# Kernel tuning notes

Measured on AMD Instinct MI355X. Metric: run time of the kernel, lower is better.

Reference implementation:

```python
import jax, jax.numpy as jnp
import numpy as np

B = 262144
L = 16      # latent_dim
H = 64      # hidden_dim
C = 8       # num_charts
O = 32      # output_dim
TAU_MIN = 0.01
TAU_DENOM_MIN = 0.001
EPS = 0.001
LN_EPS = 1e-5


def setup_inputs() -> dict:
    key = jax.random.key(0)
    ks = jax.random.split(key, 16)
    # latents kept well inside the Poincare ball
    z_geo = 0.1 * jax.random.normal(ks[0], (B, L), dtype=jnp.float32)
    z_tex = 0.1 * jax.random.normal(ks[1], (B, L), dtype=jnp.float32)
    def lin(k, fan_in, shape):
        bound = 1.0 / np.sqrt(fan_in)
        return jax.random.uniform(k, shape, jnp.float32, -bound, bound)
    chart_w = lin(ks[2], L, (C, H, L))   # stacked per-chart Linear weights
    chart_b = lin(ks[3], L, (C, H))
    router_w = lin(ks[4], L, (C, L))
    router_b = lin(ks[5], L, (C,))
    centers = 0.02 * jax.random.normal(ks[6], (C, L), dtype=jnp.float32)
    tex_w = lin(ks[7], L, (H, L))
    tex_b = lin(ks[8], L, (H,))
    ln_g = jnp.ones((H,), jnp.float32)
    ln_b = jnp.zeros((H,), jnp.float32)
    w1 = lin(ks[9], H, (H, H))
    b1 = lin(ks[10], H, (H,))
    w2 = lin(ks[11], H, (O, H))
    b2 = lin(ks[12], H, (O,))
    return dict(z_geo=z_geo, z_tex=z_tex, chart_w=chart_w, chart_b=chart_b,
                router_w=router_w, router_b=router_b, centers=centers,
                tex_w=tex_w, tex_b=tex_b, ln_g=ln_g, ln_b=ln_b,
                w1=w1, b1=b1, w2=w2, b2=b2)


def _temperature(z):
    r2 = jnp.sum(z * z, axis=-1)                      # [B]
    denom = jnp.maximum(1.0 - r2, TAU_DENOM_MIN)
    tau = (np.sqrt(L) * denom) * 0.5
    return jnp.maximum(tau, TAU_MIN)                  # [B]


def _gelu(x):
    return jax.nn.gelu(x, approximate=False)


def reference(z_geo, z_tex, chart_w, chart_b, router_w, router_b, centers,
              tex_w, tex_b, ln_g, ln_b, w1, b1, w2, b2):
    # hyperbolic distance scores  [B, C]
    diff = z_geo[:, None, :] - centers[None, :, :]
    dist_sq = jnp.sum(diff * diff, axis=-1)
    z_sq = jnp.sum(z_geo * z_geo, axis=-1, keepdims=True)   # [B,1]
    c_sq = jnp.sum(centers * centers, axis=-1)[None, :]      # [1,C]
    denom = (1.0 - z_sq) * (1.0 - c_sq)
    arg = 1.0 + 2.0 * dist_sq / (denom + EPS)
    dist = jnp.arccosh(jnp.maximum(arg, 1.0 + EPS))
    tau = _temperature(z_geo)                                # [B]
    scores = -dist / tau[:, None]
    scores = scores + 0.1 * (z_geo @ router_w.T + router_b) / tau[:, None]
    router_weights = jax.nn.softmax(scores, axis=-1)         # [B,C]

    # dense chart projection + weighted blend
    h_stack = jnp.einsum('bl,chl->bch', z_geo, chart_w) + chart_b[None]  # [B,C,H]
    h_global = jnp.sum(h_stack * router_weights[:, :, None], axis=1)     # [B,H]
    h_tex = z_tex @ tex_w.T + tex_b
    h = h_global + h_tex

    # renderer: LayerNorm -> GELU -> Linear -> GELU -> Linear
    mu = jnp.mean(h, axis=-1, keepdims=True)
    var = jnp.mean((h - mu) ** 2, axis=-1, keepdims=True)
    hn = (h - mu) * jax.lax.rsqrt(var + LN_EPS) * ln_g + ln_b
    h1 = _gelu(_gelu(hn) @ w1.T + b1)
    x_hat = h1 @ w2.T + b2
    return x_hat, router_weights
```

## Files before the change

### kernel.cpp

```cpp
#include <hip/hip_runtime.h>
#include <hip/hip_bf16.h>
#include <hip/hip_fp16.h>


typedef __attribute__((ext_vector_type(8))) short short8;
typedef __attribute__((ext_vector_type(4))) float f32x4;

__device__ __forceinline__ int pkbf2(float a, float b) {
    union { __hip_bfloat162 h2; int i; } u;
    u.h2 = __float22bfloat162_rn(make_float2(a, b));
    return u.i;
}
__device__ __forceinline__ short pkbf1(float a) { return (short)pkbf2(a, 0.f); }

__device__ __forceinline__ float gelu_fast(float x) {
    float x2 = x * x;
    float t  = __expf(fmaf(x2, 0.07135481f, 1.5957691f) * x);
    float r  = __builtin_amdgcn_rcpf(t + 1.0f);
    return fmaf(-x, r, x);
}
__device__ __forceinline__ int bpack(int k, int n, int KT) {
    return (((n >> 4) * KT + (k >> 5)) * 64 + (n & 15) + (((k & 31) >> 3) << 4)) * 8 + (k & 7);
}
__device__ __forceinline__ int gswz(int g) {
    return g ^ (((g >> 4) & 3) << 1) ^ ((g >> 3) & 1);
}
__device__ __forceinline__ short8 packrow8(const float* base) {
    const float4* p = (const float4*)base;
    float4 a = p[0], b = p[1];
    union { short8 s; int i[4]; } f;
    f.i[0] = pkbf2(a.x, a.y); f.i[1] = pkbf2(a.z, a.w);
    f.i[2] = pkbf2(b.x, b.y); f.i[3] = pkbf2(b.z, b.w);
    return f.s;
}

__global__ void pack_weights(const float* __restrict__ cw, const float* __restrict__ cb,
                             const float* __restrict__ txw, const float* __restrict__ txb,
                             const float* __restrict__ w1,  const float* __restrict__ w2,
                             const float* __restrict__ cen, const float* __restrict__ rb,
                             short* __restrict__ ws)
{
    const int tid = threadIdx.x;
    const int b = blockIdx.x;
    if (b < 40) {
        int idx = b * 256 + tid;
        int k = idx >> 6, n = idx & 63;
        float v;
        if (k < 128)       v = cw[(k >> 4) * 1024 + n * 16 + (k & 15)];
        else if (k < 144)  v = txw[n * 16 + (k - 128)];
        else if (k < 152)  v = cb[(k - 144) * 64 + n];
        else if (k == 152) v = txb[n];
        else               v = 0.f;
        ws[bpack(k, n, 5)] = pkbf1(v);
    } else if (b == 40) {
        for (int f = tid; f < 512; f += 256) {
            int lane = f & 63, e = f >> 6;
            int nt = e >> 1, kt = e & 1;
            int col = lane & 15, qq = lane >> 4;
            *(short8*)(ws + 10240 + f * 8) =
                packrow8(w1 + (nt * 16 + col) * 64 + kt * 32 + qq * 8);
        }
    } else if (b == 41) {
        int f = tid;
        int lane = f & 63, e = f >> 6;
        int nt = e >> 1, kt = e & 1;
        int col = lane & 15, qq = lane >> 4;
        *(short8*)(ws + 14336 + f * 8) =
            packrow8(w2 + (nt * 16 + col) * 64 + kt * 32 + qq * 8);
    } else {
        if (tid < 8) {
            float csq = 0.f;
            for (int l = 0; l < 16; l++) { float cv = cen[tid * 16 + l]; csq = fmaf(cv, cv, csq); }
            ((float4*)((char*)ws + 32768))[tid] =
                make_float4(csq, 1.0f - csq, 0.1f * rb[tid], 0.f);
        }
    }
}

constexpr int SCR_OFF = 20480;
constexpr int RS_OFF  = 28672;
constexpr int W2L_OFF = 32768;
constexpr int SMEM_SZ = 36864;

__global__ __launch_bounds__(256, 4) void topo_mfma(
    const float* __restrict__ zg,  const float* __restrict__ ztx,
    const float* __restrict__ cw,  const float* __restrict__ cb,
    const float* __restrict__ rw,  const float* __restrict__ rb,
    const float* __restrict__ cen, const float* __restrict__ txw,
    const float* __restrict__ txb, const float* __restrict__ lng,
    const float* __restrict__ lnb, const float* __restrict__ w1,
    const float* __restrict__ b1,  const float* __restrict__ w2,
    const float* __restrict__ b2,  const short* __restrict__ wsp,
    const int prepacked,
    float* __restrict__ out, int Btot)
{
    __shared__ __align__(16) char smem[SMEM_SZ];
    short* WA = (short*)smem;
    __half* RSh = (__half*)(smem + RS_OFF);
    const short8* W2L = (const short8*)(smem + W2L_OFF);

    const int tid = threadIdx.x;
    const int wv = tid >> 6, lane = tid & 63;
    const int q = lane >> 4, col = lane & 15;
    const int sub = (lane >> 3) & 1, j = lane & 7;

    if (prepacked) {
        const int4* src = (const int4*)wsp;
        int4* dst = (int4*)smem;
        #pragma unroll
        for (int i = 0; i < 5; i++) dst[i * 256 + tid] = src[i * 256 + tid];
        ((int4*)(smem + W2L_OFF))[tid] = ((const int4*)((const char*)wsp + 28672))[tid];
    } else {
        for (int idx = tid; idx < 160 * 64; idx += 256) {
            int k = idx >> 6, n = idx & 63;
            float v;
            if (k < 128)       v = cw[(k >> 4) * 1024 + n * 16 + (k & 15)];
            else if (k < 144)  v = txw[n * 16 + (k - 128)];
            else if (k < 152)  v = cb[(k - 144) * 64 + n];
            else if (k == 152) v = txb[n];
            else               v = 0.f;
            WA[bpack(k, n, 5)] = pkbf1(v);
        }
        {
            int e = tid >> 6, ln = tid & 63;
            int nt = e >> 1, kt = e & 1;
            *(short8*)(smem + W2L_OFF + (e * 64 + ln) * 16) =
                packrow8(w2 + (nt * 16 + (ln & 15)) * 64 + kt * 32 + (ln >> 4) * 8);
        }
    }

    const long sG = (long)blockIdx.x * 256 + tid;
    {
        float z[16];
        const float4* pg = (const float4*)(zg + sG * 16);
        #pragma unroll
        for (int v = 0; v < 4; v++) {
            float4 a = pg[v];
            z[v*4+0]=a.x; z[v*4+1]=a.y; z[v*4+2]=a.z; z[v*4+3]=a.w;
        }
        float r2 = 0.f;
        #pragma unroll
        for (int l = 0; l < 16; l++) r2 = fmaf(z[l], z[l], r2);
        const float inv_tau = __builtin_amdgcn_rcpf(fmaxf(2.0f * fmaxf(1.0f - r2, 0.001f), 0.01f));
        const float omr2 = 1.0f - r2;
        const float4* cvp = (const float4*)((const char*)wsp + 32768);
        float scv[8]; float smax = -1e30f;
        #pragma unroll
        for (int c = 0; c < 8; c++) {
            float csq, omc2, rb1;
            if (prepacked) {
                float4 kv = cvp[c]; csq = kv.x; omc2 = kv.y; rb1 = kv.z;
            } else {
                csq = 0.f;
                #pragma unroll
                for (int l = 0; l < 16; l++) { float cv = cen[c*16+l]; csq = fmaf(cv, cv, csq); }
                omc2 = 1.0f - csq; rb1 = 0.1f * rb[c];
            }
            const float4* cp = (const float4*)(cen + c * 16);
            const float4* rp = (const float4*)(rw  + c * 16);
            float zc = 0.f, dotv = 0.f;
            #pragma unroll
            for (int v = 0; v < 4; v++) {
                float4 cv = cp[v], rv = rp[v];
                zc   = fmaf(z[v*4+0],cv.x, fmaf(z[v*4+1],cv.y,
                       fmaf(z[v*4+2],cv.z, fmaf(z[v*4+3],cv.w, zc))));
                dotv = fmaf(z[v*4+0],rv.x, fmaf(z[v*4+1],rv.y,
                       fmaf(z[v*4+2],rv.z, fmaf(z[v*4+3],rv.w, dotv))));
            }
            float dsq = fmaf(-2.0f, zc, r2 + csq);
            float u = 2.0f * dsq * __builtin_amdgcn_rcpf(omr2 * omc2 + 0.001f);
            u = fmaxf(u, 0.001f);
            float dist  = __logf((1.0f + u) + __builtin_amdgcn_sqrtf(u * (u + 2.0f)));
            float score = (fmaf(0.1f, dotv, rb1) - dist) * inv_tau;
            scv[c] = score; smax = fmaxf(smax, score);
        }
        float esum = 0.f;
        #pragma unroll
        for (int c = 0; c < 8; c++) { scv[c] = __expf(scv[c] - smax); esum += scv[c]; }
        const float rinv = __builtin_amdgcn_rcpf(esum);
        union { ushort us[8]; int4 v; } hv;
        #pragma unroll
        for (int c = 0; c < 8; c++) {
            scv[c] *= rinv;
            hv.us[(c & 1) * 4 + (c >> 1)] = __half_as_ushort(__float2half_rn(scv[c]));
        }
        *(int4*)(RSh + tid * 8) = hv.v;
        float4* pr = (float4*)(out + (long)Btot * 32 + sG * 8);
        pr[0] = make_float4(scv[0], scv[1], scv[2], scv[3]);
        pr[1] = make_float4(scv[4], scv[5], scv[6], scv[7]);
    }

    short8 W1F[4][2];
    if (prepacked) {
        const short8* p1 = (const short8*)(wsp + 10240);
        #pragma unroll
        for (int nt = 0; nt < 4; nt++)
            #pragma unroll
            for (int kt = 0; kt < 2; kt++)
                W1F[nt][kt] = p1[(nt * 2 + kt) * 64 + lane];
    } else {
        const int kb = q * 8;
        #pragma unroll
        for (int nt = 0; nt < 4; nt++)
            #pragma unroll
            for (int kt = 0; kt < 2; kt++)
                W1F[nt][kt] = packrow8(w1 + (nt * 16 + col) * 64 + kt * 32 + kb);
    }
    float lngv[4], lnbv[4], b1v[4], b2v[2];
    #pragma unroll
    for (int nt = 0; nt < 4; nt++) {
        lngv[nt] = lng[nt * 16 + col];
        lnbv[nt] = lnb[nt * 16 + col];
        b1v[nt]  = b1[nt * 16 + col];
    }
    b2v[0] = b2[col]; b2v[1] = b2[16 + col];

    __syncthreads();

    short* scr = (short*)(smem + SCR_OFF) + wv * 1024;
    union Frag { short8 s; int i[4]; };

    const long blockBase = (long)blockIdx.x * 256;
    const float* zrow = zg  + (blockBase + wv * 64 + col) * 16 + ((q & 1) << 3);
    const float* trow = ztx + (blockBase + wv * 64 + col) * 16 + ((q & 1) << 3);

    float4 za = ((const float4*)zrow)[0], zb = ((const float4*)zrow)[1];
    float4 ta = ((const float4*)trow)[0], tb = ((const float4*)trow)[1];

    for (int t = 0; t < 4; t++) {
        const int  mBase = wv * 64 + t * 16;
        const int  sL = mBase + col;
        const int  rsb = sL * 8;

        float rc[4];
        {
            union { unsigned long long u; __half2 h[2]; } rr;
            rr.u = *(const unsigned long long*)(RSh + rsb + ((q >> 1) << 2));
            float2 f0 = __half22float2(rr.h[0]);
            float2 f1 = __half22float2(rr.h[1]);
            rc[0] = f0.x; rc[1] = f0.y; rc[2] = f1.x; rc[3] = f1.y;
        }

        f32x4 acc[4] = {{0.f,0.f,0.f,0.f},{0.f,0.f,0.f,0.f},{0.f,0.f,0.f,0.f},{0.f,0.f,0.f,0.f}};
        __builtin_amdgcn_s_setprio(1);
        #pragma unroll
        for (int kt = 0; kt < 4; kt++) {
            float r = rc[kt];
            Frag f;
            f.i[0] = pkbf2(r * za.x, r * za.y);
            f.i[1] = pkbf2(r * za.z, r * za.w);
            f.i[2] = pkbf2(r * zb.x, r * zb.y);
            f.i[3] = pkbf2(r * zb.z, r * zb.w);
            #pragma unroll
            for (int nt = 0; nt < 4; nt++) {
                short8 bf = *(const short8*)(WA + (nt * 5 + kt) * 512 + lane * 8);
                acc[nt] = __builtin_amdgcn_mfma_f32_16x16x32_bf16(f.s, bf, acc[nt], 0, 0, 0);
            }
        }
        {
            Frag f;
            if (q < 2) {
                f.i[0] = pkbf2(ta.x, ta.y); f.i[1] = pkbf2(ta.z, ta.w);
                f.i[2] = pkbf2(tb.x, tb.y); f.i[3] = pkbf2(tb.z, tb.w);
            } else if (q == 2) {
                union { int4 u; __half2 h[4]; } rv;
                rv.u = *(const int4*)(RSh + rsb);
                float2 e0 = __half22float2(rv.h[0]);
                float2 e1 = __half22float2(rv.h[1]);
                float2 e2 = __half22float2(rv.h[2]);
                float2 e3 = __half22float2(rv.h[3]);
                f.i[0] = pkbf2(e0.x, e2.x);
                f.i[1] = pkbf2(e0.y, e2.y);
                f.i[2] = pkbf2(e1.x, e3.x);
                f.i[3] = pkbf2(e1.y, e3.y);
            } else {
                f.i[0] = pkbf2(1.0f, 0.f); f.i[1] = 0; f.i[2] = 0; f.i[3] = 0;
            }
            #pragma unroll
            for (int nt = 0; nt < 4; nt++) {
                short8 bf = *(const short8*)(WA + (nt * 5 + 4) * 512 + lane * 8);
                acc[nt] = __builtin_amdgcn_mfma_f32_16x16x32_bf16(f.s, bf, acc[nt], 0, 0, 0);
            }
        }
        __builtin_amdgcn_s_setprio(0);

        if (t < 3) {
            const float4* pzn = (const float4*)(zrow + (t + 1) * 256);
            const float4* ptn = (const float4*)(trow + (t + 1) * 256);
            za = pzn[0]; zb = pzn[1]; ta = ptn[0]; tb = ptn[1];
        }

        float mu[4], rsd[4];
        #pragma unroll
        for (int reg = 0; reg < 4; reg++) {
            float a = acc[0][reg], b = acc[1][reg], c = acc[2][reg], d = acc[3][reg];
            float s  = (a + b) + (c + d);
            float s2 = fmaf(a, a, fmaf(b, b, fmaf(c, c, d * d)));
            s  += __shfl_xor(s, 1);  s  += __shfl_xor(s, 2);
            s  += __shfl_xor(s, 4);  s  += __shfl_xor(s, 8);
            s2 += __shfl_xor(s2, 1); s2 += __shfl_xor(s2, 2);
            s2 += __shfl_xor(s2, 4); s2 += __shfl_xor(s2, 8);
            float m = s * (1.0f / 64.0f);
            mu[reg]  = m;
            rsd[reg] = rsqrtf(fmaf(s2, 1.0f / 64.0f, -m * m) + 1e-5f);
        }

        #pragma unroll
        for (int nt = 0; nt < 4; nt++) {
            int high = (nt & 1) * 2 + sub;
            #pragma unroll
            for (int reg = 0; reg < 4; reg++) {
                float hn = (acc[nt][reg] - mu[reg]) * rsd[reg] * lngv[nt] + lnbv[nt];
                int grp = gswz((q * 4 + reg) + 16 * high);
                scr[(nt >> 1) * 512 + grp * 8 + j] = pkbf1(gelu_fast(hn));
            }
        }
        asm volatile("s_waitcnt lgkmcnt(0)" ::: "memory");

        short8 A2[2];
        {
            int grp = gswz(lane);
            A2[0] = *(const short8*)(scr +       grp * 8);
            A2[1] = *(const short8*)(scr + 512 + grp * 8);
        }

        #pragma unroll
        for (int nt = 0; nt < 4; nt++) {
            f32x4 a2 = {0.f, 0.f, 0.f, 0.f};
            __builtin_amdgcn_s_setprio(1);
            a2 = __builtin_amdgcn_mfma_f32_16x16x32_bf16(A2[0], W1F[nt][0], a2, 0, 0, 0);
            a2 = __builtin_amdgcn_mfma_f32_16x16x32_bf16(A2[1], W1F[nt][1], a2, 0, 0, 0);
            __builtin_amdgcn_s_setprio(0);
            int high = (nt & 1) * 2 + sub;
            #pragma unroll
            for (int reg = 0; reg < 4; reg++) {
                float h1v = gelu_fast(a2[reg] + b1v[nt]);
                int grp = gswz((q * 4 + reg) + 16 * high);
                scr[(nt >> 1) * 512 + grp * 8 + j] = pkbf1(h1v);
            }
        }
        asm volatile("s_waitcnt lgkmcnt(0)" ::: "memory");

        short8 A3[2];
        {
            int grp = gswz(lane);
            A3[0] = *(const short8*)(scr +       grp * 8);
            A3[1] = *(const short8*)(scr + 512 + grp * 8);
        }

        const long sOutBase = blockBase + mBase + q * 4;
        #pragma unroll
        for (int nt = 0; nt < 2; nt++) {
            f32x4 a3 = {0.f, 0.f, 0.f, 0.f};
            short8 wA = W2L[(nt * 2 + 0) * 64 + lane];
            short8 wB = W2L[(nt * 2 + 1) * 64 + lane];
            __builtin_amdgcn_s_setprio(1);
            a3 = __builtin_amdgcn_mfma_f32_16x16x32_bf16(A3[0], wA, a3, 0, 0, 0);
            a3 = __builtin_amdgcn_mfma_f32_16x16x32_bf16(A3[1], wB, a3, 0, 0, 0);
            __builtin_amdgcn_s_setprio(0);
            #pragma unroll
            for (int reg = 0; reg < 4; reg++)
                out[(sOutBase + reg) * 32 + nt * 16 + col] = a3[reg] + b2v[nt];
        }
    }
}

extern "C" void kernel_launch(void* const* d_in, const int* in_sizes, int n_in,
                              void* d_out, int out_size, void* d_ws, size_t ws_size,
                              hipStream_t stream) {
    const int B = in_sizes[0] / 16;
    const int prepacked = (d_ws != nullptr && ws_size >= 32896) ? 1 : 0;
    if (prepacked) {
        hipLaunchKernelGGL(pack_weights, dim3(43), dim3(256), 0, stream,
            (const float*)d_in[2],  (const float*)d_in[3],
            (const float*)d_in[7],  (const float*)d_in[8],
            (const float*)d_in[11], (const float*)d_in[13],
            (const float*)d_in[6],  (const float*)d_in[5],
            (short*)d_ws);
    }
    dim3 grid(B / 256), block(256);
    hipLaunchKernelGGL(topo_mfma, grid, block, 0, stream,
        (const float*)d_in[0],  (const float*)d_in[1],
        (const float*)d_in[2],  (const float*)d_in[3],
        (const float*)d_in[4],  (const float*)d_in[5],
        (const float*)d_in[6],  (const float*)d_in[7],
        (const float*)d_in[8],  (const float*)d_in[9],
        (const float*)d_in[10], (const float*)d_in[11],
        (const float*)d_in[12], (const float*)d_in[13],
        (const float*)d_in[14],
        (const short*)d_ws, prepacked,
        (float*)d_out, B);
}
```

Before: 138.9 us.

## Pass router weights via wave shuffles instead of LDS, raise occupancy to 5

Each thread keeps its packed fp16 router weights in registers, and the MFMA tile loop fetches them from the owning lane with __shfl instead of reading a shared-memory staging buffer. This removes 4 KB of LDS, so shared memory shrinks to 32 KB and launch bounds ask for 5 blocks per CU. It also drops the s_setprio hints around the MFMA groups. The tighter register budget at 5 waves per SIMD risks spills, and the shuffles add cross-lane instructions in place of LDS reads.

```diff
diff --git a/kernel.cpp b/kernel.cpp
--- a/kernel.cpp
+++ b/kernel.cpp
@@ -78,11 +78,10 @@
 }
 
 constexpr int SCR_OFF = 20480;
-constexpr int RS_OFF  = 28672;
-constexpr int W2L_OFF = 32768;
-constexpr int SMEM_SZ = 36864;
-
-__global__ __launch_bounds__(256, 4) void topo_mfma(
+constexpr int W2L_OFF = 28672;
+constexpr int SMEM_SZ = 32768;
+
+__global__ __launch_bounds__(256, 5) void topo_mfma(
     const float* __restrict__ zg,  const float* __restrict__ ztx,
     const float* __restrict__ cw,  const float* __restrict__ cb,
     const float* __restrict__ rw,  const float* __restrict__ rb,
@@ -96,7 +95,6 @@
 {
     __shared__ __align__(16) char smem[SMEM_SZ];
     short* WA = (short*)smem;
-    __half* RSh = (__half*)(smem + RS_OFF);
     const short8* W2L = (const short8*)(smem + W2L_OFF);
 
     const int tid = threadIdx.x;
@@ -130,6 +128,7 @@
     }
 
     const long sG = (long)blockIdx.x * 256 + tid;
+    int4 rsh;
     {
         float z[16];
         const float4* pg = (const float4*)(zg + sG * 16);
@@ -184,7 +183,7 @@
             scv[c] *= rinv;
             hv.us[(c & 1) * 4 + (c >> 1)] = __half_as_ushort(__float2half_rn(scv[c]));
         }
-        *(int4*)(RSh + tid * 8) = hv.v;
+        rsh = hv.v;
         float4* pr = (float4*)(out + (long)Btot * 32 + sG * 8);
         pr[0] = make_float4(scv[0], scv[1], scv[2], scv[3]);
         pr[1] = make_float4(scv[4], scv[5], scv[6], scv[7]);
@@ -229,20 +228,24 @@
 
     for (int t = 0; t < 4; t++) {
         const int  mBase = wv * 64 + t * 16;
-        const int  sL = mBase + col;
-        const int  rsb = sL * 8;
+        const int  srcLn = t * 16 + col;
+
+        int4 got;
+        got.x = __shfl(rsh.x, srcLn);
+        got.y = __shfl(rsh.y, srcLn);
+        got.z = __shfl(rsh.z, srcLn);
+        got.w = __shfl(rsh.w, srcLn);
 
         float rc[4];
         {
-            union { unsigned long long u; __half2 h[2]; } rr;
-            rr.u = *(const unsigned long long*)(RSh + rsb + ((q >> 1) << 2));
-            float2 f0 = __half22float2(rr.h[0]);
-            float2 f1 = __half22float2(rr.h[1]);
+            int w0 = (q < 2) ? got.x : got.z;
+            int w1s = (q < 2) ? got.y : got.w;
+            float2 f0 = __half22float2(*(__half2*)&w0);
+            float2 f1 = __half22float2(*(__half2*)&w1s);
             rc[0] = f0.x; rc[1] = f0.y; rc[2] = f1.x; rc[3] = f1.y;
         }
 
         f32x4 acc[4] = {{0.f,0.f,0.f,0.f},{0.f,0.f,0.f,0.f},{0.f,0.f,0.f,0.f},{0.f,0.f,0.f,0.f}};
-        __builtin_amdgcn_s_setprio(1);
         #pragma unroll
         for (int kt = 0; kt < 4; kt++) {
             float r = rc[kt];
@@ -263,12 +266,10 @@
                 f.i[0] = pkbf2(ta.x, ta.y); f.i[1] = pkbf2(ta.z, ta.w);
                 f.i[2] = pkbf2(tb.x, tb.y); f.i[3] = pkbf2(tb.z, tb.w);
             } else if (q == 2) {
-                union { int4 u; __half2 h[4]; } rv;
-                rv.u = *(const int4*)(RSh + rsb);
-                float2 e0 = __half22float2(rv.h[0]);
-                float2 e1 = __half22float2(rv.h[1]);
-                float2 e2 = __half22float2(rv.h[2]);
-                float2 e3 = __half22float2(rv.h[3]);
+                float2 e0 = __half22float2(*(__half2*)&got.x);
+                float2 e1 = __half22float2(*(__half2*)&got.y);
+                float2 e2 = __half22float2(*(__half2*)&got.z);
+                float2 e3 = __half22float2(*(__half2*)&got.w);
                 f.i[0] = pkbf2(e0.x, e2.x);
                 f.i[1] = pkbf2(e0.y, e2.y);
                 f.i[2] = pkbf2(e1.x, e3.x);
@@ -282,7 +283,6 @@
                 acc[nt] = __builtin_amdgcn_mfma_f32_16x16x32_bf16(f.s, bf, acc[nt], 0, 0, 0);
             }
         }
-        __builtin_amdgcn_s_setprio(0);
 
         if (t < 3) {
             const float4* pzn = (const float4*)(zrow + (t + 1) * 256);
@@ -327,10 +327,8 @@
         #pragma unroll
         for (int nt = 0; nt < 4; nt++) {
             f32x4 a2 = {0.f, 0.f, 0.f, 0.f};
-            __builtin_amdgcn_s_setprio(1);
             a2 = __builtin_amdgcn_mfma_f32_16x16x32_bf16(A2[0], W1F[nt][0], a2, 0, 0, 0);
             a2 = __builtin_amdgcn_mfma_f32_16x16x32_bf16(A2[1], W1F[nt][1], a2, 0, 0, 0);
-            __builtin_amdgcn_s_setprio(0);
             int high = (nt & 1) * 2 + sub;
             #pragma unroll
             for (int reg = 0; reg < 4; reg++) {
@@ -354,10 +352,8 @@
             f32x4 a3 = {0.f, 0.f, 0.f, 0.f};
             short8 wA = W2L[(nt * 2 + 0) * 64 + lane];
             short8 wB = W2L[(nt * 2 + 1) * 64 + lane];
-            __builtin_amdgcn_s_setprio(1);
             a3 = __builtin_amdgcn_mfma_f32_16x16x32_bf16(A3[0], wA, a3, 0, 0, 0);
             a3 = __builtin_amdgcn_mfma_f32_16x16x32_bf16(A3[1], wB, a3, 0, 0, 0);
-            __builtin_amdgcn_s_setprio(0);
             #pragma unroll
             for (int reg = 0; reg < 4; reg++)
                 out[(sOutBase + reg) * 32 + nt * 16 + col] = a3[reg] + b2v[nt];
```

Result: slower. 162.0 us (+16.7%).
